# Kernel optimization log

Hardware: AMD Instinct MI355X
Metric: run time of the kernel (lower is better)

## Reference

```python
import jax, jax.numpy as jnp
import numpy as np
from jax import lax

N_QUBITS = 8
DIM = 256  # 2**8 amplitudes
NUM_BLOCKS = 16
DEPTH = 1
ALPHA = 0.5
BATCH = 512

# Z-sign tables: qubit 0 is the most-significant bit of the flattened state index
_bits = (np.arange(DIM)[:, None] >> (N_QUBITS - 1 - np.arange(N_QUBITS))) & 1  # (256, 8)
_SIGNS = jnp.asarray(1.0 - 2.0 * _bits, dtype=jnp.float32)  # (256, 8)
_pairs = [(i, j) for i in range(N_QUBITS) for j in range(i + 1, N_QUBITS)]
_PAIR_SIGNS = jnp.stack([_SIGNS[:, i] * _SIGNS[:, j] for (i, j) in _pairs], axis=1)  # (256, 28)


def _apply_ry(state, c, s, q):
    # state: (N, 256) real (RY and CNOT keep the state real); gate on qubit q
    dl, dr = 2 ** q, 2 ** (N_QUBITS - 1 - q)
    st = state.reshape(-1, dl, 2, dr)
    s0, s1 = st[:, :, 0, :], st[:, :, 1, :]
    c_, s_ = c[:, None, None], s[:, None, None]
    n0 = c_ * s0 - s_ * s1
    n1 = s_ * s0 + c_ * s1
    return jnp.stack([n0, n1], axis=2).reshape(-1, DIM)


def _apply_cnot_chain(state, i):
    # CNOT control=i, target=i+1 (adjacent qubits)
    dl, dr = 2 ** i, 2 ** (N_QUBITS - 2 - i)
    st = state.reshape(-1, dl, 2, 2, dr)
    c0 = st[:, :, 0]                  # control=0: unchanged
    c1 = st[:, :, 1][:, :, ::-1]      # control=1: flip target bit
    return jnp.stack([c0, c1], axis=2).reshape(-1, DIM)


def _quantum_map(theta):
    # theta: (N, 8) -> (N, 36) [Z_i expectations (8) then Z_i Z_j for i<j (28)]
    half = 0.5 * theta
    c, s = jnp.cos(half), jnp.sin(half)
    state = jnp.zeros((theta.shape[0], DIM), dtype=theta.dtype).at[:, 0].set(1.0)
    for q in range(N_QUBITS):
        state = _apply_ry(state, c[:, q], s[:, q], q)
    for _ in range(DEPTH):
        for i in range(N_QUBITS - 1):
            state = _apply_cnot_chain(state, i)
    p = state * state  # probabilities (state is real)
    single = p @ _SIGNS          # (N, 8)
    two_body = p @ _PAIR_SIGNS   # (N, 28)
    return jnp.concatenate([single, two_body], axis=1)


def _bn(x, g, b, m, v):
    # inference-mode BatchNorm2d, eps=1e-5
    inv = g / jnp.sqrt(v + 1e-5)
    return x * inv[None, :, None, None] + (b - m * inv)[None, :, None, None]


def _conv(x, w, b):
    y = lax.conv_general_dilated(x, w, (1, 1), 'SAME',
                                 dimension_numbers=('NCHW', 'OIHW', 'NCHW'))
    return y + b[None, :, None, None]


def _maxpool2(x):
    return lax.reduce_window(x, -jnp.inf, lax.max, (1, 1, 2, 2), (1, 1, 2, 2), 'VALID')


def setup_inputs() -> dict:
    key = jax.random.key(0)
    ks = jax.random.split(key, 8)
    f32 = jnp.float32
    return {
        'x': jax.random.normal(ks[0], (BATCH, 3, 64, 64), dtype=f32),
        'conv1_w': jax.random.normal(ks[1], (16, 3, 3, 3), dtype=f32) * 0.1,
        'conv1_b': jnp.zeros((16,), f32),
        'bn1_g': jnp.ones((16,), f32), 'bn1_b': jnp.zeros((16,), f32),
        'bn1_m': jnp.zeros((16,), f32), 'bn1_v': jnp.ones((16,), f32),
        'conv2_w': jax.random.normal(ks[2], (32, 16, 3, 3), dtype=f32) * 0.08,
        'conv2_b': jnp.zeros((32,), f32),
        'bn2_g': jnp.ones((32,), f32), 'bn2_b': jnp.zeros((32,), f32),
        'bn2_m': jnp.zeros((32,), f32), 'bn2_v': jnp.ones((32,), f32),
        'conv3_w': jax.random.normal(ks[3], (64, 32, 3, 3), dtype=f32) * 0.06,
        'conv3_b': jnp.zeros((64,), f32),
        'bn3_g': jnp.ones((64,), f32), 'bn3_b': jnp.zeros((64,), f32),
        'bn3_m': jnp.zeros((64,), f32), 'bn3_v': jnp.ones((64,), f32),
        'proj_w': jax.random.normal(ks[4], (NUM_BLOCKS, 256, N_QUBITS), dtype=f32) * 0.06,
        'proj_b': jnp.zeros((NUM_BLOCKS, N_QUBITS), f32),
        'cls_w': jax.random.normal(ks[5], (10, NUM_BLOCKS * 36), dtype=f32) * 0.04,
        'cls_b': jnp.zeros((10,), f32),
    }


def reference(x, conv1_w, conv1_b, bn1_g, bn1_b, bn1_m, bn1_v,
              conv2_w, conv2_b, bn2_g, bn2_b, bn2_m, bn2_v,
              conv3_w, conv3_b, bn3_g, bn3_b, bn3_m, bn3_v,
              proj_w, proj_b, cls_w, cls_b):
    h = _maxpool2(jax.nn.relu(_bn(_conv(x, conv1_w, conv1_b), bn1_g, bn1_b, bn1_m, bn1_v)))
    h = _maxpool2(jax.nn.relu(_bn(_conv(h, conv2_w, conv2_b), bn2_g, bn2_b, bn2_m, bn2_v)))
    h = _maxpool2(jax.nn.relu(_bn(_conv(h, conv3_w, conv3_b), bn3_g, bn3_b, bn3_m, bn3_v)))
    B = h.shape[0]
    feats = h.reshape(B, NUM_BLOCKS, 256)  # 16 chunks of 256
    z = jnp.einsum('bkc,kcd->bkd', feats, proj_w) + proj_b[None]  # (B, 16, 8)
    theta = ALPHA * jnp.tanh(z)
    q_out = _quantum_map(theta.reshape(B * NUM_BLOCKS, N_QUBITS))  # (B*16, 36)
    combined = q_out.reshape(B, NUM_BLOCKS * 36)
    return combined @ cls_w.T + cls_b
```

## Files before the change

### kernel.cpp

```cpp
#include <hip/hip_runtime.h>
#include <hip/hip_bf16.h>
#include <math.h>

typedef __attribute__((ext_vector_type(8))) short short8;
typedef __attribute__((ext_vector_type(4))) float f32x4;

__device__ __forceinline__ unsigned short f2bf(float f) {
    union { float f; unsigned u; } x; x.f = f;
    unsigned r = x.u + 0x7FFF + ((x.u >> 16) & 1);
    return (unsigned short)(r >> 16);
}

__device__ __forceinline__ short8 mk8(uint2 a, uint2 b) {
    union { uint2 u[2]; short8 s; } x;
    x.u[0] = a; x.u[1] = b;
    return x.s;
}

__global__ void k_prep(const float* __restrict__ w2, const float* __restrict__ w3,
    const float* g2, const float* be2, const float* m2, const float* v2, const float* cb2,
    const float* g3, const float* be3, const float* m3, const float* v3, const float* cb3,
    const float* __restrict__ w1,
    const float* g1, const float* be1, const float* m1, const float* v1, const float* cb1,
    const float* __restrict__ pjw,
    unsigned short* __restrict__ wp2, unsigned short* __restrict__ wp3,
    unsigned short* __restrict__ wp1,
    float* __restrict__ cst2, float* __restrict__ cst3, float* __restrict__ cst1,
    float* __restrict__ pjwt)
{
    int tid = blockIdx.x * 256 + threadIdx.x;
    if (tid < 5120) {
        int j = tid & 7, lane = (tid >> 3) & 63, o = (tid >> 9) & 1, s = tid >> 10;
        int kl = ((lane >> 4) << 3) + j;
        int tp = s * 2 + (kl >> 4);
        int ic = kl & 15;
        int oc = o * 16 + (lane & 15);
        float val = (tp < 9) ? w2[(oc * 16 + ic) * 9 + tp] : 0.f;
        wp2[tid] = f2bf(val);
    } else if (tid < 23552) {
        int idx = tid - 5120;
        int j = idx & 7, lane = (idx >> 3) & 63, o = (idx >> 9) & 3, tap = idx >> 11;
        int ic = ((lane >> 4) << 3) + j;
        int oc = o * 16 + (lane & 15);
        wp3[idx] = f2bf(w3[(oc * 32 + ic) * 9 + tap]);
    } else if (tid < 23648) {
        int c = tid - 23552;
        if (c < 32) {
            float inv = g2[c] * rsqrtf(v2[c] + 1e-5f);
            cst2[c] = inv;
            cst2[32 + c] = (cb2[c] - m2[c]) * inv + be2[c];
        } else {
            int c3 = c - 32;
            float inv = g3[c3] * rsqrtf(v3[c3] + 1e-5f);
            cst3[c3] = inv;
            cst3[64 + c3] = (cb3[c3] - m3[c3]) * inv + be3[c3];
        }
    } else if (tid < 24672) {
        int idx = tid - 23648;
        int j = idx & 7, lane = (idx >> 3) & 63, s = (idx >> 9) & 1;
        int k = ((lane >> 4) << 3) + j;
        int oc = lane & 15;
        float val = 0.f;
        if (s == 0) {
            int tap = k >> 2, ic = k & 3;
            if (ic < 3) val = w1[(oc * 3 + ic) * 9 + tap];
        } else {
            if (k < 3) val = w1[(oc * 3 + k) * 9 + 8];
        }
        wp1[idx] = f2bf(val);
    } else if (tid < 24688) {
        int c = tid - 24672;
        float inv = g1[c] * rsqrtf(v1[c] + 1e-5f);
        cst1[c] = inv;
        cst1[16 + c] = (cb1[c] - m1[c]) * inv + be1[c];
    } else if (tid < 57456) {
        int idx = tid - 24688;
        int k = idx >> 11, d = (idx >> 8) & 7, c = idx & 255;
        pjwt[idx] = pjw[k * 2048 + c * 8 + d];
    }
}

__global__ __launch_bounds__(256) void k_conv1m(const float* __restrict__ x,
    const unsigned short* __restrict__ wp, const float* __restrict__ cst,
    unsigned short* __restrict__ out)
{
    __shared__ __align__(16) unsigned short xs[2244 * 4];
    int bid = blockIdx.x;
    int b = bid >> 1, h = bid & 1;
    int t = threadIdx.x;
    const float* img = x + (size_t)b * 3 * 4096;
    int y0 = h * 32 - 1;
    #pragma unroll 1
    for (int i = 0; i < 9; ++i) {
        int idx = t + i * 256;
        if (idx < 2244) {
            int y = idx / 66, xx = idx - y * 66;
            int gy = y0 + y, gx = xx - 1;
            float v0 = 0.f, v1 = 0.f, v2 = 0.f;
            if ((unsigned)gy < 64u && (unsigned)gx < 64u) {
                const float* pb = img + gy * 64 + gx;
                v0 = pb[0]; v1 = pb[4096]; v2 = pb[8192];
            }
            uint2 pk;
            pk.x = (unsigned)f2bf(v0) | ((unsigned)f2bf(v1) << 16);
            pk.y = (unsigned)f2bf(v2);
            ((uint2*)xs)[idx] = pk;
        }
    }
    int lane = t & 63, w = t >> 6;
    int q = lane >> 4, xl = lane & 15;
    short8 A0 = *(const short8*)(wp + (lane << 3));
    short8 A1 = *(const short8*)(wp + ((64 + lane) << 3));
    int t0 = 2 * q, t1 = 2 * q + 1;
    int dy0 = t0 / 3 - 1, dx0 = t0 % 3 - 1;
    int dy1 = t1 / 3 - 1, dx1 = t1 % 3 - 1;
    float invr[4], bsr[4];
    #pragma unroll
    for (int reg = 0; reg < 4; ++reg) {
        int oc = q * 4 + reg;
        invr[reg] = cst[oc]; bsr[reg] = cst[16 + oc];
    }
    __syncthreads();
    #pragma unroll 1
    for (int xT = 0; xT < 4; ++xT) {
        int xb = xT * 16 + xl + 1;
        float pv[4];
        #pragma unroll
        for (int r = 0; r < 8; ++r) {
            int ly = w * 8 + r + 1;
            const uint2* base = (const uint2*)xs;
            uint2 ua = base[(ly + dy0) * 66 + xb + dx0];
            uint2 ub = base[(ly + dy1) * 66 + xb + dx1];
            uint2 uc = base[(ly + 1) * 66 + xb + 1];
            f32x4 acc = (f32x4){0.f, 0.f, 0.f, 0.f};
            acc = __builtin_amdgcn_mfma_f32_16x16x32_bf16(A0, mk8(ua, ub), acc, 0, 0, 0);
            acc = __builtin_amdgcn_mfma_f32_16x16x32_bf16(A1, mk8(uc, uc), acc, 0, 0, 0);
            #pragma unroll
            for (int reg = 0; reg < 4; ++reg) {
                float val = fmaxf(acc[reg] * invr[reg] + bsr[reg], 0.f);
                if (r & 1) {
                    float vm = fmaxf(val, pv[reg]);
                    float vo = fmaxf(vm, __shfl_xor(vm, 1, 64));
                    if (!(lane & 1)) {
                        int oc = q * 4 + reg;
                        int py = h * 16 + w * 4 + (r >> 1);
                        int px = xT * 8 + (xl >> 1);
                        out[(((size_t)b * 32 + py) * 32 + px) * 16 + oc] = f2bf(vo);
                    }
                } else {
                    pv[reg] = val;
                }
            }
        }
    }
}

__global__ __launch_bounds__(256) void k_conv2m(const unsigned short* __restrict__ in,
    const unsigned short* __restrict__ wp, const float* __restrict__ cst,
    unsigned short* __restrict__ out)
{
    __shared__ __align__(16) unsigned short x2[612 * 24];
    int bid = blockIdx.x;
    int b = bid >> 1, h = bid & 1;
    int t = threadIdx.x;
    const unsigned short* src = in + (size_t)b * 16384;
    #pragma unroll 1
    for (int i = 0; i < 5; ++i) {
        int idx = t + i * 256;
        if (idx < 1224) {
            int pos = idx >> 1, half = idx & 1;
            int y = pos / 34, xx = pos - y * 34;
            int gy = h * 16 + y - 1, gx = xx - 1;
            uint4 val = {0u, 0u, 0u, 0u};
            if ((unsigned)gy < 32u && (unsigned)gx < 32u)
                val = *(const uint4*)(src + (gy * 32 + gx) * 16 + half * 8);
            *(uint4*)(x2 + pos * 24 + half * 8) = val;
        }
    }
    int lane = t & 63, w = t >> 6;
    int q = lane >> 4, xl = lane & 15;
    short8 A[5][2];
    #pragma unroll
    for (int s = 0; s < 5; ++s)
        #pragma unroll
        for (int o = 0; o < 2; ++o)
            A[s][o] = *(const short8*)(wp + (((s * 2 + o) * 64 + lane) << 3));
    int dyA[5], dxA[5];
    #pragma unroll
    for (int s = 0; s < 5; ++s) {
        int tp = s * 2 + (q >> 1); if (tp > 8) tp = 8;
        int d3 = tp / 3;
        dyA[s] = d3 - 1; dxA[s] = tp - d3 * 3 - 1;
    }
    __syncthreads();
    f32x4 acc[4][2][2];
    #pragma unroll
    for (int r = 0; r < 4; ++r)
        #pragma unroll
        for (int xT = 0; xT < 2; ++xT)
            #pragma unroll
            for (int o = 0; o < 2; ++o)
                acc[r][xT][o] = (f32x4){0.f, 0.f, 0.f, 0.f};
    #pragma unroll
    for (int r = 0; r < 4; ++r) {
        int ry = w * 4 + r + 1;
        #pragma unroll
        for (int xT = 0; xT < 2; ++xT) {
            int xb = xT * 16 + xl + 1;
            #pragma unroll
            for (int s = 0; s < 5; ++s) {
                int pos = (ry + dyA[s]) * 34 + xb + dxA[s];
                short8 B = *(const short8*)(x2 + pos * 24 + (q & 1) * 8);
                acc[r][xT][0] = __builtin_amdgcn_mfma_f32_16x16x32_bf16(A[s][0], B, acc[r][xT][0], 0, 0, 0);
                acc[r][xT][1] = __builtin_amdgcn_mfma_f32_16x16x32_bf16(A[s][1], B, acc[r][xT][1], 0, 0, 0);
            }
        }
    }
    #pragma unroll
    for (int oT = 0; oT < 2; ++oT) {
        #pragma unroll
        for (int reg = 0; reg < 4; ++reg) {
            int oc = oT * 16 + q * 4 + reg;
            float inv = cst[oc], bs = cst[32 + oc];
            #pragma unroll
            for (int rp = 0; rp < 2; ++rp) {
                #pragma unroll
                for (int xT = 0; xT < 2; ++xT) {
                    float v0 = fmaxf(acc[rp * 2][xT][oT][reg] * inv + bs, 0.f);
                    float v1 = fmaxf(acc[rp * 2 + 1][xT][oT][reg] * inv + bs, 0.f);
                    float vm = fmaxf(v0, v1);
                    float vo = fmaxf(vm, __shfl_xor(vm, 1, 64));
                    if (!(lane & 1)) {
                        int py = h * 8 + w * 2 + rp;
                        int px = xT * 8 + (xl >> 1);
                        out[(((size_t)b * 16 + py) * 16 + px) * 32 + oc] = f2bf(vo);
                    }
                }
            }
        }
    }
}

__global__ __launch_bounds__(256) void k_conv3h(const unsigned short* __restrict__ in,
    const unsigned short* __restrict__ wp, const float* __restrict__ cst,
    const float* __restrict__ pjwt, const float* __restrict__ pjb,
    const float* __restrict__ cw, const float* __restrict__ cbias,
    float* __restrict__ out)
{
    __shared__ __align__(16) unsigned short x3[324 * 40];
    __shared__ __align__(16) float feats[64][68];
    __shared__ float czs[16][8];
    __shared__ float part[16][10];
    int b = blockIdx.x;
    int t = threadIdx.x;
    const unsigned short* src = in + (size_t)b * 8192;
    #pragma unroll 1
    for (int i = 0; i < 6; ++i) {
        int idx = t + i * 256;
        if (idx < 1296) {
            int pos = idx >> 2, qt = idx & 3;
            int y = pos / 18, xx = pos - y * 18;
            int gy = y - 1, gx = xx - 1;
            uint4 val = {0u, 0u, 0u, 0u};
            if ((unsigned)gy < 16u && (unsigned)gx < 16u)
                val = *(const uint4*)(src + (gy * 16 + gx) * 32 + qt * 8);
            *(uint4*)(x3 + pos * 40 + qt * 8) = val;
        }
    }
    __syncthreads();
    int lane = t & 63, w = t >> 6;
    int q = lane >> 4, xl = lane & 15;
    #pragma unroll 1
    for (int op = 0; op < 2; ++op) {
        short8 A[9][2];
        #pragma unroll
        for (int tap = 0; tap < 9; ++tap)
            #pragma unroll
            for (int tt = 0; tt < 2; ++tt)
                A[tap][tt] = *(const short8*)(wp + (((tap * 4 + op * 2 + tt) * 64 + lane) << 3));
        f32x4 acc[4][2];
        #pragma unroll
        for (int r = 0; r < 4; ++r) {
            acc[r][0] = (f32x4){0.f, 0.f, 0.f, 0.f};
            acc[r][1] = (f32x4){0.f, 0.f, 0.f, 0.f};
        }
        #pragma unroll
        for (int r = 0; r < 4; ++r) {
            int ry = w * 4 + r + 1;
            #pragma unroll
            for (int tap = 0; tap < 9; ++tap) {
                int pos = (ry + tap / 3 - 1) * 18 + xl + (tap % 3);
                short8 B = *(const short8*)(x3 + pos * 40 + q * 8);
                acc[r][0] = __builtin_amdgcn_mfma_f32_16x16x32_bf16(A[tap][0], B, acc[r][0], 0, 0, 0);
                acc[r][1] = __builtin_amdgcn_mfma_f32_16x16x32_bf16(A[tap][1], B, acc[r][1], 0, 0, 0);
            }
        }
        #pragma unroll
        for (int tt = 0; tt < 2; ++tt) {
            #pragma unroll
            for (int reg = 0; reg < 4; ++reg) {
                int oc = (op * 2 + tt) * 16 + q * 4 + reg;
                float inv = cst[oc], bs = cst[64 + oc];
                #pragma unroll
                for (int rp = 0; rp < 2; ++rp) {
                    float v0 = fmaxf(acc[rp * 2][tt][reg] * inv + bs, 0.f);
                    float v1 = fmaxf(acc[rp * 2 + 1][tt][reg] * inv + bs, 0.f);
                    float vm = fmaxf(v0, v1);
                    float vo = fmaxf(vm, __shfl_xor(vm, 1, 64));
                    if (!(lane & 1))
                        feats[oc][(w * 2 + rp) * 8 + (xl >> 1)] = vo;
                }
            }
        }
    }
    __syncthreads();
    if (t < 128) {
        int k = t >> 3, d = t & 7;
        const float4* wrow = (const float4*)(pjwt + (k * 8 + d) * 256);
        float zacc = 0.f;
        #pragma unroll 4
        for (int c4 = 0; c4 < 64; ++c4) {
            float4 wv = wrow[c4];
            float4 fv = *(const float4*)(&feats[k * 4 + (c4 >> 4)][4 * (c4 & 15)]);
            zacc = fmaf(wv.x, fv.x, zacc);
            zacc = fmaf(wv.y, fv.y, zacc);
            zacc = fmaf(wv.z, fv.z, zacc);
            zacc = fmaf(wv.w, fv.w, zacc);
        }
        float z = zacc + pjb[k * 8 + d];
        czs[k][d] = cosf(0.5f * tanhf(z));
    }
    __syncthreads();
    if (t < 160) {
        int k = t / 10, c = t - (t / 10) * 10;
        float cz[8];
        #pragma unroll
        for (int i = 0; i < 8; ++i) cz[i] = czs[k][i];
        const float* cwp = cw + c * 576 + k * 36;
        float s = 0.f;
        float pp = 1.f;
        #pragma unroll
        for (int i = 0; i < 8; ++i) { pp *= cz[i]; s = fmaf(pp, cwp[i], s); }
        int cnt = 8;
        #pragma unroll
        for (int i = 0; i < 8; ++i) {
            float p2 = 1.f;
            #pragma unroll
            for (int j = i + 1; j < 8; ++j) { p2 *= cz[j]; s = fmaf(p2, cwp[cnt++], s); }
        }
        part[k][c] = s;
    }
    __syncthreads();
    if (t < 10) {
        float s = cbias[t];
        #pragma unroll
        for (int k = 0; k < 16; ++k) s += part[k][t];
        out[b * 10 + t] = s;
    }
}

extern "C" void kernel_launch(void* const* d_in, const int* in_sizes, int n_in,
                              void* d_out, int out_size, void* d_ws, size_t ws_size,
                              hipStream_t stream) {
    const float* x     = (const float*)d_in[0];
    const float* c1w   = (const float*)d_in[1];
    const float* c1b   = (const float*)d_in[2];
    const float* b1g   = (const float*)d_in[3];
    const float* b1b   = (const float*)d_in[4];
    const float* b1m   = (const float*)d_in[5];
    const float* b1v   = (const float*)d_in[6];
    const float* c2w   = (const float*)d_in[7];
    const float* c2b   = (const float*)d_in[8];
    const float* b2g   = (const float*)d_in[9];
    const float* b2b   = (const float*)d_in[10];
    const float* b2m   = (const float*)d_in[11];
    const float* b2v   = (const float*)d_in[12];
    const float* c3w   = (const float*)d_in[13];
    const float* c3b   = (const float*)d_in[14];
    const float* b3g   = (const float*)d_in[15];
    const float* b3b   = (const float*)d_in[16];
    const float* b3m   = (const float*)d_in[17];
    const float* b3v   = (const float*)d_in[18];
    const float* pjw   = (const float*)d_in[19];
    const float* pjb   = (const float*)d_in[20];
    const float* cw    = (const float*)d_in[21];
    const float* cbias = (const float*)d_in[22];
    float* outp = (float*)d_out;

    unsigned short* h1 = (unsigned short*)d_ws;
    unsigned short* h2 = h1 + 8388608;
    unsigned char* prep = (unsigned char*)(h2 + 4194304);
    unsigned short* wp2 = (unsigned short*)prep;
    unsigned short* wp3 = (unsigned short*)(prep + 16384);
    unsigned short* wp1 = (unsigned short*)(prep + 16384 + 36864);
    float* cst2 = (float*)(prep + 16384 + 36864 + 2048);
    float* cst3 = cst2 + 64;
    float* cst1 = cst3 + 128;
    float* pjwt = (float*)(prep + 16384 + 36864 + 2048 + 1024);

    k_prep<<<225, 256, 0, stream>>>(c2w, c3w, b2g, b2b, b2m, b2v, c2b,
                                    b3g, b3b, b3m, b3v, c3b,
                                    c1w, b1g, b1b, b1m, b1v, c1b, pjw,
                                    wp2, wp3, wp1, cst2, cst3, cst1, pjwt);
    k_conv1m<<<1024, 256, 0, stream>>>(x, wp1, cst1, h1);
    k_conv2m<<<1024, 256, 0, stream>>>(h1, wp2, cst2, h2);
    k_conv3h<<<512, 256, 0, stream>>>(h2, wp3, cst3, pjwt, pjb, cw, cbias, outp);
}
```

Baseline: 164.5 us.

## Fuse all three conv stages and head into one per-image kernel

```diff
diff --git a/kernel.cpp b/kernel.cpp
--- a/kernel.cpp
+++ b/kernel.cpp
@@ -14,6 +14,12 @@
 __device__ __forceinline__ short8 mk8(uint2 a, uint2 b) {
     union { uint2 u[2]; short8 s; } x;
     x.u[0] = a; x.u[1] = b;
+    return x.s;
+}
+
+__device__ __forceinline__ short8 mk8u(unsigned a, unsigned b, unsigned c, unsigned d) {
+    union { unsigned u[4]; short8 s; } x;
+    x.u[0] = a; x.u[1] = b; x.u[2] = c; x.u[3] = d;
     return x.s;
 }
 
@@ -80,111 +86,114 @@
     }
 }
 
-__global__ __launch_bounds__(256) void k_conv1m(const float* __restrict__ x,
-    const unsigned short* __restrict__ wp, const float* __restrict__ cst,
-    unsigned short* __restrict__ out)
+__global__ __launch_bounds__(256, 2) void k_fused(
+    const float* __restrict__ x,
+    const unsigned short* __restrict__ wp1, const float* __restrict__ cst1,
+    const unsigned short* __restrict__ wp2, const float* __restrict__ cst2,
+    const unsigned short* __restrict__ wp3, const float* __restrict__ cst3,
+    const float* __restrict__ pjwt, const float* __restrict__ pjb,
+    const float* __restrict__ cw, const float* __restrict__ cbias,
+    float* __restrict__ out)
 {
-    __shared__ __align__(16) unsigned short xs[2244 * 4];
-    int bid = blockIdx.x;
-    int b = bid >> 1, h = bid & 1;
-    int t = threadIdx.x;
-    const float* img = x + (size_t)b * 3 * 4096;
-    int y0 = h * 32 - 1;
-    #pragma unroll 1
-    for (int i = 0; i < 9; ++i) {
-        int idx = t + i * 256;
-        if (idx < 2244) {
-            int y = idx / 66, xx = idx - y * 66;
-            int gy = y0 + y, gx = xx - 1;
-            float v0 = 0.f, v1 = 0.f, v2 = 0.f;
-            if ((unsigned)gy < 64u && (unsigned)gx < 64u) {
-                const float* pb = img + gy * 64 + gx;
-                v0 = pb[0]; v1 = pb[4096]; v2 = pb[8192];
-            }
-            uint2 pk;
-            pk.x = (unsigned)f2bf(v0) | ((unsigned)f2bf(v1) << 16);
-            pk.y = (unsigned)f2bf(v2);
-            ((uint2*)xs)[idx] = pk;
-        }
-    }
-    int lane = t & 63, w = t >> 6;
-    int q = lane >> 4, xl = lane & 15;
-    short8 A0 = *(const short8*)(wp + (lane << 3));
-    short8 A1 = *(const short8*)(wp + ((64 + lane) << 3));
+    __shared__ __align__(16) unsigned char smem[62784];
+    unsigned short* xs  = (unsigned short*)smem;
+    unsigned short* h2t = (unsigned short*)smem;
+    unsigned short* h1  = (unsigned short*)(smem + 25920);
+    float* feats = (float*)(smem + 25920);
+    float* czs   = (float*)(smem + 25920 + 17408);
+    float* partl = czs + 128;
+
+    int b = blockIdx.x, t = threadIdx.x;
+    int lane = t & 63, w = t >> 6, q = lane >> 4, xl = lane & 15;
+    const float* img = x + (size_t)b * 12288;
+
+    short8 A10 = *(const short8*)(wp1 + (lane << 3));
+    short8 A11 = *(const short8*)(wp1 + ((64 + lane) << 3));
     int t0 = 2 * q, t1 = 2 * q + 1;
     int dy0 = t0 / 3 - 1, dx0 = t0 % 3 - 1;
     int dy1 = t1 / 3 - 1, dx1 = t1 % 3 - 1;
-    float invr[4], bsr[4];
+    float inv1[4], bs1[4];
     #pragma unroll
     for (int reg = 0; reg < 4; ++reg) {
-        int oc = q * 4 + reg;
-        invr[reg] = cst[oc]; bsr[reg] = cst[16 + oc];
-    }
-    __syncthreads();
+        inv1[reg] = cst1[q * 4 + reg];
+        bs1[reg]  = cst1[16 + q * 4 + reg];
+    }
     #pragma unroll 1
-    for (int xT = 0; xT < 4; ++xT) {
-        int xb = xT * 16 + xl + 1;
-        float pv[4];
-        #pragma unroll
-        for (int r = 0; r < 8; ++r) {
-            int ly = w * 8 + r + 1;
-            const uint2* base = (const uint2*)xs;
-            uint2 ua = base[(ly + dy0) * 66 + xb + dx0];
-            uint2 ub = base[(ly + dy1) * 66 + xb + dx1];
-            uint2 uc = base[(ly + 1) * 66 + xb + 1];
-            f32x4 acc = (f32x4){0.f, 0.f, 0.f, 0.f};
-            acc = __builtin_amdgcn_mfma_f32_16x16x32_bf16(A0, mk8(ua, ub), acc, 0, 0, 0);
-            acc = __builtin_amdgcn_mfma_f32_16x16x32_bf16(A1, mk8(uc, uc), acc, 0, 0, 0);
-            #pragma unroll
-            for (int reg = 0; reg < 4; ++reg) {
-                float val = fmaxf(acc[reg] * invr[reg] + bsr[reg], 0.f);
-                if (r & 1) {
-                    float vm = fmaxf(val, pv[reg]);
-                    float vo = fmaxf(vm, __shfl_xor(vm, 1, 64));
-                    if (!(lane & 1)) {
-                        int oc = q * 4 + reg;
-                        int py = h * 16 + w * 4 + (r >> 1);
-                        int px = xT * 8 + (xl >> 1);
-                        out[(((size_t)b * 32 + py) * 32 + px) * 16 + oc] = f2bf(vo);
+    for (int h = 0; h < 2; ++h) {
+        if (h) __syncthreads();
+        int y0 = h * 32 - 1;
+        #pragma unroll 1
+        for (int i = 0; i < 9; ++i) {
+            int idx = t + i * 256;
+            if (idx < 2244) {
+                int y = idx / 66, xx = idx - y * 66;
+                int gy = y0 + y, gx = xx - 1;
+                float v0 = 0.f, v1 = 0.f, v2 = 0.f;
+                if ((unsigned)gy < 64u && (unsigned)gx < 64u) {
+                    const float* pb = img + gy * 64 + gx;
+                    v0 = pb[0]; v1 = pb[4096]; v2 = pb[8192];
+                }
+                uint2 pk;
+                pk.x = (unsigned)f2bf(v0) | ((unsigned)f2bf(v1) << 16);
+                pk.y = (unsigned)f2bf(v2);
+                ((uint2*)xs)[idx] = pk;
+            }
+        }
+        __syncthreads();
+        #pragma unroll 1
+        for (int xT = 0; xT < 4; ++xT) {
+            int xb = xT * 16 + xl + 1;
+            float pv[4], vo[4];
+            #pragma unroll
+            for (int r = 0; r < 8; ++r) {
+                int ly = w * 8 + r + 1;
+                const uint2* base = (const uint2*)xs;
+                uint2 ua = base[(ly + dy0) * 66 + xb + dx0];
+                uint2 ub = base[(ly + dy1) * 66 + xb + dx1];
+                uint2 uc = base[(ly + 1) * 66 + xb + 1];
+                f32x4 acc = (f32x4){0.f, 0.f, 0.f, 0.f};
+                acc = __builtin_amdgcn_mfma_f32_16x16x32_bf16(A10, mk8(ua, ub), acc, 0, 0, 0);
+                acc = __builtin_amdgcn_mfma_f32_16x16x32_bf16(A11, mk8(uc, uc), acc, 0, 0, 0);
+                #pragma unroll
+                for (int reg = 0; reg < 4; ++reg) {
+                    float val = fmaxf(acc[reg] * inv1[reg] + bs1[reg], 0.f);
+                    if (r & 1) {
+                        float vm = fmaxf(val, pv[reg]);
+                        vo[reg] = fmaxf(vm, __shfl_xor(vm, 1, 64));
+                    } else {
+                        pv[reg] = val;
                     }
-                } else {
-                    pv[reg] = val;
-                }
-            }
-        }
-    }
-}
-
-__global__ __launch_bounds__(256) void k_conv2m(const unsigned short* __restrict__ in,
-    const unsigned short* __restrict__ wp, const float* __restrict__ cst,
-    unsigned short* __restrict__ out)
-{
-    __shared__ __align__(16) unsigned short x2[612 * 24];
-    int bid = blockIdx.x;
-    int b = bid >> 1, h = bid & 1;
-    int t = threadIdx.x;
-    const unsigned short* src = in + (size_t)b * 16384;
-    #pragma unroll 1
-    for (int i = 0; i < 5; ++i) {
-        int idx = t + i * 256;
-        if (idx < 1224) {
-            int pos = idx >> 1, half = idx & 1;
-            int y = pos / 34, xx = pos - y * 34;
-            int gy = h * 16 + y - 1, gx = xx - 1;
-            uint4 val = {0u, 0u, 0u, 0u};
-            if ((unsigned)gy < 32u && (unsigned)gx < 32u)
-                val = *(const uint4*)(src + (gy * 32 + gx) * 16 + half * 8);
-            *(uint4*)(x2 + pos * 24 + half * 8) = val;
-        }
-    }
-    int lane = t & 63, w = t >> 6;
-    int q = lane >> 4, xl = lane & 15;
-    short8 A[5][2];
+                }
+                if ((r & 1) && !(lane & 1)) {
+                    int py = h * 16 + w * 4 + (r >> 1);
+                    int px = xT * 8 + (xl >> 1);
+                    int pos = py * 32 + px;
+                    unsigned u0 = (unsigned)f2bf(vo[0]) | ((unsigned)f2bf(vo[1]) << 16);
+                    unsigned u1 = (unsigned)f2bf(vo[2]) | ((unsigned)f2bf(vo[3]) << 16);
+                    unsigned* hp = (unsigned*)h1 + pos * 9 + q * 2;
+                    hp[0] = u0; hp[1] = u1;
+                }
+            }
+        }
+    }
+    __syncthreads();
+
+    if (t < 68) {
+        int y, xx;
+        if (t < 18)      { y = 0;       xx = t; }
+        else if (t < 36) { y = 17;      xx = t - 18; }
+        else if (t < 52) { y = t - 35;  xx = 0; }
+        else             { y = t - 51;  xx = 17; }
+        uint4* p = (uint4*)(h2t + (y * 18 + xx) * 40);
+        uint4 z = {0u, 0u, 0u, 0u};
+        p[0] = z; p[1] = z; p[2] = z; p[3] = z; p[4] = z;
+    }
+    short8 A2[5][2];
     #pragma unroll
     for (int s = 0; s < 5; ++s)
         #pragma unroll
         for (int o = 0; o < 2; ++o)
-            A[s][o] = *(const short8*)(wp + (((s * 2 + o) * 64 + lane) << 3));
+            A2[s][o] = *(const short8*)(wp2 + (((s * 2 + o) * 64 + lane) << 3));
     int dyA[5], dxA[5];
     #pragma unroll
     for (int s = 0; s < 5; ++s) {
@@ -192,92 +201,73 @@
         int d3 = tp / 3;
         dyA[s] = d3 - 1; dxA[s] = tp - d3 * 3 - 1;
     }
-    __syncthreads();
-    f32x4 acc[4][2][2];
-    #pragma unroll
-    for (int r = 0; r < 4; ++r)
-        #pragma unroll
-        for (int xT = 0; xT < 2; ++xT)
-            #pragma unroll
-            for (int o = 0; o < 2; ++o)
-                acc[r][xT][o] = (f32x4){0.f, 0.f, 0.f, 0.f};
-    #pragma unroll
-    for (int r = 0; r < 4; ++r) {
-        int ry = w * 4 + r + 1;
-        #pragma unroll
-        for (int xT = 0; xT < 2; ++xT) {
-            int xb = xT * 16 + xl + 1;
-            #pragma unroll
-            for (int s = 0; s < 5; ++s) {
-                int pos = (ry + dyA[s]) * 34 + xb + dxA[s];
-                short8 B = *(const short8*)(x2 + pos * 24 + (q & 1) * 8);
-                acc[r][xT][0] = __builtin_amdgcn_mfma_f32_16x16x32_bf16(A[s][0], B, acc[r][xT][0], 0, 0, 0);
-                acc[r][xT][1] = __builtin_amdgcn_mfma_f32_16x16x32_bf16(A[s][1], B, acc[r][xT][1], 0, 0, 0);
-            }
-        }
-    }
-    #pragma unroll
-    for (int oT = 0; oT < 2; ++oT) {
-        #pragma unroll
-        for (int reg = 0; reg < 4; ++reg) {
-            int oc = oT * 16 + q * 4 + reg;
-            float inv = cst[oc], bs = cst[32 + oc];
-            #pragma unroll
-            for (int rp = 0; rp < 2; ++rp) {
+    #pragma unroll 1
+    for (int rr = 0; rr < 2; ++rr) {
+        f32x4 acc[4][2][2];
+        #pragma unroll
+        for (int r = 0; r < 4; ++r)
+            #pragma unroll
+            for (int xT = 0; xT < 2; ++xT)
+                #pragma unroll
+                for (int o = 0; o < 2; ++o)
+                    acc[r][xT][o] = (f32x4){0.f, 0.f, 0.f, 0.f};
+        #pragma unroll
+        for (int r = 0; r < 4; ++r) {
+            int ry = w * 8 + rr * 4 + r;
+            #pragma unroll
+            for (int xT = 0; xT < 2; ++xT) {
+                int gxb = xT * 16 + xl;
+                #pragma unroll
+                for (int s = 0; s < 5; ++s) {
+                    int gy = ry + dyA[s], gx = gxb + dxA[s];
+                    bool ok = ((unsigned)gy < 32u) && ((unsigned)gx < 32u);
+                    int pos = ok ? gy * 32 + gx : 0;
+                    const unsigned* hp = (const unsigned*)h1 + pos * 9 + (q & 1) * 4;
+                    unsigned u0 = hp[0], u1 = hp[1], u2 = hp[2], u3 = hp[3];
+                    if (!ok) { u0 = 0; u1 = 0; u2 = 0; u3 = 0; }
+                    short8 B = mk8u(u0, u1, u2, u3);
+                    acc[r][xT][0] = __builtin_amdgcn_mfma_f32_16x16x32_bf16(A2[s][0], B, acc[r][xT][0], 0, 0, 0);
+                    acc[r][xT][1] = __builtin_amdgcn_mfma_f32_16x16x32_bf16(A2[s][1], B, acc[r][xT][1], 0, 0, 0);
+                }
+            }
+        }
+        #pragma unroll
+        for (int oT = 0; oT < 2; ++oT)
+            #pragma unroll
+            for (int rp = 0; rp < 2; ++rp)
                 #pragma unroll
                 for (int xT = 0; xT < 2; ++xT) {
-                    float v0 = fmaxf(acc[rp * 2][xT][oT][reg] * inv + bs, 0.f);
-                    float v1 = fmaxf(acc[rp * 2 + 1][xT][oT][reg] * inv + bs, 0.f);
-                    float vm = fmaxf(v0, v1);
-                    float vo = fmaxf(vm, __shfl_xor(vm, 1, 64));
+                    float vo[4];
+                    #pragma unroll
+                    for (int reg = 0; reg < 4; ++reg) {
+                        int oc = oT * 16 + q * 4 + reg;
+                        float inv = cst2[oc], bs = cst2[32 + oc];
+                        float v0 = fmaxf(acc[rp * 2][xT][oT][reg] * inv + bs, 0.f);
+                        float v1 = fmaxf(acc[rp * 2 + 1][xT][oT][reg] * inv + bs, 0.f);
+                        float vm = fmaxf(v0, v1);
+                        vo[reg] = fmaxf(vm, __shfl_xor(vm, 1, 64));
+                    }
                     if (!(lane & 1)) {
-                        int py = h * 8 + w * 2 + rp;
+                        int py = w * 4 + rr * 2 + rp;
                         int px = xT * 8 + (xl >> 1);
-                        out[(((size_t)b * 16 + py) * 16 + px) * 32 + oc] = f2bf(vo);
+                        int pos = (py + 1) * 18 + (px + 1);
+                        unsigned u0 = (unsigned)f2bf(vo[0]) | ((unsigned)f2bf(vo[1]) << 16);
+                        unsigned u1 = (unsigned)f2bf(vo[2]) | ((unsigned)f2bf(vo[3]) << 16);
+                        unsigned* hp = (unsigned*)h2t + pos * 20 + oT * 8 + q * 2;
+                        hp[0] = u0; hp[1] = u1;
                     }
                 }
-            }
-        }
-    }
-}
-
-__global__ __launch_bounds__(256) void k_conv3h(const unsigned short* __restrict__ in,
-    const unsigned short* __restrict__ wp, const float* __restrict__ cst,
-    const float* __restrict__ pjwt, const float* __restrict__ pjb,
-    const float* __restrict__ cw, const float* __restrict__ cbias,
-    float* __restrict__ out)
-{
-    __shared__ __align__(16) unsigned short x3[324 * 40];
-    __shared__ __align__(16) float feats[64][68];
-    __shared__ float czs[16][8];
-    __shared__ float part[16][10];
-    int b = blockIdx.x;
-    int t = threadIdx.x;
-    const unsigned short* src = in + (size_t)b * 8192;
-    #pragma unroll 1
-    for (int i = 0; i < 6; ++i) {
-        int idx = t + i * 256;
-        if (idx < 1296) {
-            int pos = idx >> 2, qt = idx & 3;
-            int y = pos / 18, xx = pos - y * 18;
-            int gy = y - 1, gx = xx - 1;
-            uint4 val = {0u, 0u, 0u, 0u};
-            if ((unsigned)gy < 16u && (unsigned)gx < 16u)
-                val = *(const uint4*)(src + (gy * 16 + gx) * 32 + qt * 8);
-            *(uint4*)(x3 + pos * 40 + qt * 8) = val;
-        }
-    }
-    __syncthreads();
-    int lane = t & 63, w = t >> 6;
-    int q = lane >> 4, xl = lane & 15;
+    }
+    __syncthreads();
+
     #pragma unroll 1
     for (int op = 0; op < 2; ++op) {
-        short8 A[9][2];
+        short8 A3[9][2];
         #pragma unroll
         for (int tap = 0; tap < 9; ++tap)
             #pragma unroll
             for (int tt = 0; tt < 2; ++tt)
-                A[tap][tt] = *(const short8*)(wp + (((tap * 4 + op * 2 + tt) * 64 + lane) << 3));
+                A3[tap][tt] = *(const short8*)(wp3 + (((tap * 4 + op * 2 + tt) * 64 + lane) << 3));
         f32x4 acc[4][2];
         #pragma unroll
         for (int r = 0; r < 4; ++r) {
@@ -290,52 +280,54 @@
             #pragma unroll
             for (int tap = 0; tap < 9; ++tap) {
                 int pos = (ry + tap / 3 - 1) * 18 + xl + (tap % 3);
-                short8 B = *(const short8*)(x3 + pos * 40 + q * 8);
-                acc[r][0] = __builtin_amdgcn_mfma_f32_16x16x32_bf16(A[tap][0], B, acc[r][0], 0, 0, 0);
-                acc[r][1] = __builtin_amdgcn_mfma_f32_16x16x32_bf16(A[tap][1], B, acc[r][1], 0, 0, 0);
-            }
-        }
-        #pragma unroll
-        for (int tt = 0; tt < 2; ++tt) {
+                short8 B = *(const short8*)(h2t + pos * 40 + q * 8);
+                acc[r][0] = __builtin_amdgcn_mfma_f32_16x16x32_bf16(A3[tap][0], B, acc[r][0], 0, 0, 0);
+                acc[r][1] = __builtin_amdgcn_mfma_f32_16x16x32_bf16(A3[tap][1], B, acc[r][1], 0, 0, 0);
+            }
+        }
+        #pragma unroll
+        for (int tt = 0; tt < 2; ++tt)
             #pragma unroll
             for (int reg = 0; reg < 4; ++reg) {
                 int oc = (op * 2 + tt) * 16 + q * 4 + reg;
-                float inv = cst[oc], bs = cst[64 + oc];
+                float inv = cst3[oc], bs = cst3[64 + oc];
                 #pragma unroll
                 for (int rp = 0; rp < 2; ++rp) {
                     float v0 = fmaxf(acc[rp * 2][tt][reg] * inv + bs, 0.f);
                     float v1 = fmaxf(acc[rp * 2 + 1][tt][reg] * inv + bs, 0.f);
                     float vm = fmaxf(v0, v1);
-                    float vo = fmaxf(vm, __shfl_xor(vm, 1, 64));
+                    float vv = fmaxf(vm, __shfl_xor(vm, 1, 64));
                     if (!(lane & 1))
-                        feats[oc][(w * 2 + rp) * 8 + (xl >> 1)] = vo;
-                }
-            }
-        }
-    }
-    __syncthreads();
+                        feats[oc * 68 + (w * 2 + rp) * 8 + (xl >> 1)] = vv;
+                }
+            }
+    }
+    __syncthreads();
+
     if (t < 128) {
         int k = t >> 3, d = t & 7;
         const float4* wrow = (const float4*)(pjwt + (k * 8 + d) * 256);
         float zacc = 0.f;
         #pragma unroll 4
-        for (int c4 = 0; c4 < 64; ++c4) {
+        for (int i = 0; i < 64; ++i) {
+            int c4 = (i + k) & 63;
             float4 wv = wrow[c4];
-            float4 fv = *(const float4*)(&feats[k * 4 + (c4 >> 4)][4 * (c4 & 15)]);
+            const float* fp = &feats[(k * 4 + (c4 >> 4)) * 68 + 4 * (c4 & 15)];
+            float4 fv = *(const float4*)fp;
             zacc = fmaf(wv.x, fv.x, zacc);
             zacc = fmaf(wv.y, fv.y, zacc);
             zacc = fmaf(wv.z, fv.z, zacc);
             zacc = fmaf(wv.w, fv.w, zacc);
         }
         float z = zacc + pjb[k * 8 + d];
-        czs[k][d] = cosf(0.5f * tanhf(z));
+        czs[k * 8 + d] = cosf(0.5f * tanhf(z));
     }
     __syncthreads();
     if (t < 160) {
         int k = t / 10, c = t - (t / 10) * 10;
         float cz[8];
         #pragma unroll
-        for (int i = 0; i < 8; ++i) cz[i] = czs[k][i];
+        for (int i = 0; i < 8; ++i) cz[i] = czs[k * 8 + i];
         const float* cwp = cw + c * 576 + k * 36;
         float s = 0.f;
         float pp = 1.f;
@@ -348,13 +340,13 @@
             #pragma unroll
             for (int j = i + 1; j < 8; ++j) { p2 *= cz[j]; s = fmaf(p2, cwp[cnt++], s); }
         }
-        part[k][c] = s;
+        partl[k * 10 + c] = s;
     }
     __syncthreads();
     if (t < 10) {
         float s = cbias[t];
         #pragma unroll
-        for (int k = 0; k < 16; ++k) s += part[k][t];
+        for (int k = 0; k < 16; ++k) s += partl[k * 10 + t];
         out[b * 10 + t] = s;
     }
 }
@@ -387,9 +379,7 @@
     const float* cbias = (const float*)d_in[22];
     float* outp = (float*)d_out;
 
-    unsigned short* h1 = (unsigned short*)d_ws;
-    unsigned short* h2 = h1 + 8388608;
-    unsigned char* prep = (unsigned char*)(h2 + 4194304);
+    unsigned char* prep = (unsigned char*)d_ws;
     unsigned short* wp2 = (unsigned short*)prep;
     unsigned short* wp3 = (unsigned short*)(prep + 16384);
     unsigned short* wp1 = (unsigned short*)(prep + 16384 + 36864);
@@ -402,7 +392,6 @@
                                     b3g, b3b, b3m, b3v, c3b,
                                     c1w, b1g, b1b, b1m, b1v, c1b, pjw,
                                     wp2, wp3, wp1, cst2, cst3, cst1, pjwt);
-    k_conv1m<<<1024, 256, 0, stream>>>(x, wp1, cst1, h1);
-    k_conv2m<<<1024, 256, 0, stream>>>(h1, wp2, cst2, h2);
-    k_conv3h<<<512, 256, 0, stream>>>(h2, wp3, cst3, pjwt, pjb, cw, cbias, outp);
-}
+    k_fused<<<512, 256, 0, stream>>>(x, wp1, cst1, wp2, cst2, wp3, cst3,
+                                     pjwt, pjb, cw, cbias, outp);
+}
```

Result: faster. 147.1 us (-10.6%).
